# Kernel optimization log

Hardware: AMD Instinct MI355X
Metric: run time of the kernel (lower is better)

## Reference

```python
import jax, jax.numpy as jnp
import numpy as np

N_NODES = 100000
N_EDGES = 600000
IN_FEAT = 128
HID = 128
N_CLASSES = 64


def setup_inputs() -> dict:
    key = jax.random.key(0)
    ks = jax.random.split(key, 24)
    inp = {}
    inp["x"] = jax.random.normal(ks[0], (N_NODES, IN_FEAT), dtype=jnp.float32)
    for i, r in enumerate(["r0", "r1"]):
        inp[f"src_{r}"] = jax.random.randint(ks[1 + 3 * i], (N_EDGES,), 0, N_NODES, dtype=jnp.int32)
        inp[f"dst_{r}"] = jax.random.randint(ks[2 + 3 * i], (N_EDGES,), 0, N_NODES, dtype=jnp.int32)
        inp[f"ew_{r}"] = jax.random.uniform(ks[3 + 3 * i], (N_EDGES,), dtype=jnp.float32)
    def glorot(k, shape):
        fan = (shape[0] + shape[1]) / 2.0
        return jax.random.normal(k, shape, dtype=jnp.float32) / jnp.sqrt(fan)
    j = 7
    for r in ["r0", "r1"]:
        inp[f"Ws0_{r}"] = glorot(ks[j], (IN_FEAT, HID)); j += 1
        inp[f"Wn0_{r}"] = glorot(ks[j], (IN_FEAT, HID)); j += 1
        inp[f"b0_{r}"] = jnp.zeros((HID,), jnp.float32)
        inp[f"Wp_{r}"] = glorot(ks[j], (HID, HID)); j += 1
        inp[f"bp_{r}"] = jnp.zeros((HID,), jnp.float32)
        inp[f"Ws1_{r}"] = glorot(ks[j], (HID, N_CLASSES)); j += 1
        inp[f"Wn1_{r}"] = glorot(ks[j], (HID, N_CLASSES)); j += 1
        inp[f"b1_{r}"] = jnp.zeros((N_CLASSES,), jnp.float32)
    return inp


def _mean_agg(feat, src, dst, ew, n_nodes):
    # edge-weighted messages, mean over in-edges (divide by in-degree as DGL does)
    msg = feat[src] * ew[:, None]                      # [E, d]
    s = jax.ops.segment_sum(msg, dst, num_segments=n_nodes)
    deg = jax.ops.segment_sum(jnp.ones_like(ew), dst, num_segments=n_nodes)
    return s / jnp.maximum(deg, 1.0)[:, None]


def _max_agg(feat, src, dst, ew, n_nodes):
    msg = feat[src] * ew[:, None]                      # [E, d]
    m = jax.ops.segment_max(msg, dst, num_segments=n_nodes)
    deg = jax.ops.segment_sum(jnp.ones_like(ew), dst, num_segments=n_nodes)
    return jnp.where(deg[:, None] > 0, m, 0.0)         # zero for isolated nodes


def reference(x, src_r0, dst_r0, ew_r0, src_r1, dst_r1, ew_r1,
              Ws0_r0, Wn0_r0, b0_r0, Ws0_r1, Wn0_r1, b0_r1,
              Wp_r0, bp_r0, Ws1_r0, Wn1_r0, b1_r0,
              Wp_r1, bp_r1, Ws1_r1, Wn1_r1, b1_r1):
    n = x.shape[0]
    # Layer 0: per-relation SAGEConv(mean), HeteroGraphConv aggregate='sum', then relu
    h = jnp.zeros((n, Wn0_r0.shape[1]), x.dtype)
    for src, dst, ew, Ws, Wn, b in [
        (src_r0, dst_r0, ew_r0, Ws0_r0, Wn0_r0, b0_r0),
        (src_r1, dst_r1, ew_r1, Ws0_r1, Wn0_r1, b0_r1),
    ]:
        agg = _mean_agg(x, src, dst, ew, n)
        h = h + x @ Ws + agg @ Wn + b
    h = jax.nn.relu(h)
    # Classifier layer: per-relation SAGEConv(pool): relu(fc_pool(h_src)) -> max-agg
    logits = jnp.zeros((n, Wn1_r0.shape[1]), x.dtype)
    for src, dst, ew, Wp, bp, Ws, Wn, b in [
        (src_r0, dst_r0, ew_r0, Wp_r0, bp_r0, Ws1_r0, Wn1_r0, b1_r0),
        (src_r1, dst_r1, ew_r1, Wp_r1, bp_r1, Ws1_r1, Wn1_r1, b1_r1),
    ]:
        hp = jax.nn.relu(h @ Wp + bp)
        agg = _max_agg(hp, src, dst, ew, n)
        logits = logits + h @ Ws + agg @ Wn + b
    return logits
```

## Files before the change

kernel.cpp:

```cpp
#include <hip/hip_runtime.h>

typedef short bf16x8 __attribute__((ext_vector_type(8)));
typedef float f32x4 __attribute__((ext_vector_type(4)));
typedef unsigned short u16;
typedef unsigned int u32;

#define NN 100000
#define NE 600000
#define PART 12500
#define ECH 4688

__device__ __forceinline__ u16 f2b(float f) {
    u32 u = __float_as_uint(f);
    return (u16)((u + 0x7FFFu + ((u >> 16) & 1u)) >> 16);
}

__global__ void fused_setup(
    const float* __restrict__ x, u16* __restrict__ xo,
    const float* __restrict__ Ws0_0, const float* __restrict__ Ws0_1,
    const float* __restrict__ Wn0_0, const float* __restrict__ Wn0_1,
    const float* __restrict__ Wp_0,  const float* __restrict__ Wp_1,
    const float* __restrict__ Ws1_0, const float* __restrict__ Ws1_1,
    const float* __restrict__ Wn1_0, const float* __restrict__ Wn1_1,
    const float* __restrict__ b0_0, const float* __restrict__ b0_1,
    const float* __restrict__ b1_0, const float* __restrict__ b1_1,
    const float* __restrict__ bp_0, const float* __restrict__ bp_1,
    u16* __restrict__ w, float* __restrict__ bsum0, float* __restrict__ bsum1,
    float* __restrict__ bpc)
{
    int bb = blockIdx.x;
    if (bb < 12500) {
        int t = bb * 256 + threadIdx.x;
        const float4 v = reinterpret_cast<const float4*>(x)[t];
        ushort4 r; r.x = f2b(v.x); r.y = f2b(v.y); r.z = f2b(v.z); r.w = f2b(v.w);
        reinterpret_cast<ushort4*>(xo)[t] = r;
    } else {
        int t = (bb - 12500) * 256 + threadIdx.x;
        if (t < 81920) {
            int m = t >> 14, u = t & 16383;
            int n = u >> 7, k = u & 127;
            float v;
            if (m == 0)      v = Ws0_0[k * 128 + n] + Ws0_1[k * 128 + n];
            else if (m == 1) v = Wn0_0[k * 128 + n];
            else if (m == 2) v = Wn0_1[k * 128 + n];
            else if (m == 3) v = Wp_0[k * 128 + n];
            else             v = Wp_1[k * 128 + n];
            w[t] = f2b(v);
        } else if (t < 106496) {
            int u = t - 81920;
            int m = u >> 13; u &= 8191;
            int n = u >> 7, k = u & 127;
            float v;
            if (m == 0)      v = Ws1_0[k * 64 + n] + Ws1_1[k * 64 + n];
            else if (m == 1) v = Wn1_0[k * 64 + n];
            else             v = Wn1_1[k * 64 + n];
            w[t] = f2b(v);
        } else if (t < 106624) {
            int i = t - 106496; bsum0[i] = b0_0[i] + b0_1[i];
        } else if (t < 106688) {
            int i = t - 106624; bsum1[i] = b1_0[i] + b1_1[i];
        } else if (t < 106944) {
            int i = t - 106688; bpc[i] = (i < 128) ? bp_0[i] : bp_1[i - 128];
        }
    }
}

__global__ __launch_bounds__(256) void deg_part(
    const int* __restrict__ d0, const int* __restrict__ d1,
    int* __restrict__ g0, int* __restrict__ g1)
{
    int part = blockIdx.x & 7;
    int sub = blockIdx.x >> 3;
    int rel = sub & 1;
    int chunk = sub >> 1;
    const int lo = part * PART, hi = lo + PART;
    const int* d = rel ? d1 : d0;
    int* g = rel ? g1 : g0;
    const int e0 = chunk * ECH;
    const int e1 = min(e0 + ECH, NE);
    for (int e = e0 + threadIdx.x; e < e1; e += 256) {
        int dd = d[e];
        if (dd >= lo && dd < hi) atomicAdd(&g[dd], 1);
    }
}

__global__ void scan_local(const int* __restrict__ deg0, const int* __restrict__ deg1,
                           int* __restrict__ offs0, int* __restrict__ offs1,
                           int* __restrict__ bsA, int* __restrict__ bsB)
{
    __shared__ int sm[1024];
    int rel = blockIdx.x >= 98;
    int blk = blockIdx.x - rel * 98;
    const int* in = rel ? deg1 : deg0;
    int* out = rel ? offs1 : offs0;
    int* bsum = rel ? bsB : bsA;
    int t = threadIdx.x;
    int i = blk * 1024 + t;
    int v = (i < NN) ? in[i] : 0;
    sm[t] = v;
    __syncthreads();
    for (int off = 1; off < 1024; off <<= 1) {
        int add = (t >= off) ? sm[t - off] : 0;
        __syncthreads();
        sm[t] += add;
        __syncthreads();
    }
    if (i < NN) out[i] = sm[t] - v;
    if (t == 1023) bsum[blk] = sm[1023];
}

__global__ void scan_bsums(int* __restrict__ bsA, int* __restrict__ bsB)
{
    __shared__ int sm[128];
    int* bsum = blockIdx.x ? bsB : bsA;
    int t = threadIdx.x;
    int v = (t < 98) ? bsum[t] : 0;
    sm[t] = v;
    __syncthreads();
    for (int off = 1; off < 128; off <<= 1) {
        int add = (t >= off) ? sm[t - off] : 0;
        __syncthreads();
        sm[t] += add;
        __syncthreads();
    }
    if (t < 98) bsum[t] = sm[t] - v;
}

__global__ void scan_add(int* __restrict__ offs0, int* __restrict__ offs1,
                         const int* __restrict__ bsA, const int* __restrict__ bsB,
                         int* __restrict__ cur0, int* __restrict__ cur1,
                         u32* __restrict__ csr0, u32* __restrict__ csr1)
{
    int rel = blockIdx.x >= 392;
    int i = (blockIdx.x - rel * 392) * 256 + threadIdx.x;
    int* offs = rel ? offs1 : offs0;
    int* cur = rel ? cur1 : cur0;
    const int* bsum = rel ? bsB : bsA;
    if (i < NN) {
        int v = offs[i] + bsum[i >> 10];
        offs[i] = v;
        cur[i] = v;
    }
    if (i == 0) offs[NN] = NE;
    if (blockIdx.x == 0 && threadIdx.x < 8) {
        csr0[NE + threadIdx.x] = 0;
        csr1[NE + threadIdx.x] = 0;
    }
}

__global__ __launch_bounds__(256) void build_csr_part(
    const int* __restrict__ src0, const int* __restrict__ dst0,
    const float* __restrict__ ew0,
    const int* __restrict__ src1, const int* __restrict__ dst1,
    const float* __restrict__ ew1,
    int* __restrict__ cur0, int* __restrict__ cur1,
    u32* __restrict__ csr0, u32* __restrict__ csr1)
{
    int part = blockIdx.x & 7;
    int sub = blockIdx.x >> 3;
    int rel = sub & 1;
    int chunk = sub >> 1;
    const int lo = part * PART, hi = lo + PART;
    const int* src = rel ? src1 : src0;
    const int* dst = rel ? dst1 : dst0;
    const float* ew = rel ? ew1 : ew0;
    int* cur = rel ? cur1 : cur0;
    u32* csr = rel ? csr1 : csr0;
    const int e0 = chunk * ECH;
    const int e1 = min(e0 + ECH, NE);
    for (int e = e0 + threadIdx.x; e < e1; e += 256) {
        int d = dst[e];
        if (d >= lo && d < hi) {
            int p = atomicAdd(&cur[d], 1);
            u32 q = (u32)__float2int_rn(ew[e] * 32767.f);
            csr[p] = ((u32)src[e] << 15) | q;
        }
    }
}

template<bool MAXAGG>
__global__ __launch_bounds__(256) void gather(
    const u16* __restrict__ F0, const u16* __restrict__ F1,
    const int* __restrict__ offs0, const u32* __restrict__ csr0, u16* __restrict__ o0,
    const int* __restrict__ offs1, const u32* __restrict__ csr1, u16* __restrict__ o1)
{
    int b = blockIdx.x;
    int rel = b >= 25000;
    const u16* F = rel ? F1 : F0;
    const int* offs = rel ? offs1 : offs0;
    const u32* csr = rel ? csr1 : csr0;
    u16* out = rel ? o1 : o0;
    int node = (b - rel * 25000) * 4 + (threadIdx.x >> 6);
    int lane = threadIdx.x & 63;
    int beg = __builtin_amdgcn_readfirstlane(offs[node]);
    int end = __builtin_amdgcn_readfirstlane(offs[node + 1]);
    const u16* base = F + (lane << 1);

    float acc0[8], acc1[8];
#pragma unroll
    for (int i = 0; i < 8; ++i) { acc0[i] = 0.f; acc1[i] = 0.f; }

    for (int e = beg; e < end; e += 8) {
        u32 E[8];
        float wq[8];
#pragma unroll
        for (int i = 0; i < 8; ++i) E[i] = csr[e + i];
        wq[0] = (float)(E[0] & 0x7FFFu);
#pragma unroll
        for (int i = 1; i < 8; ++i)
            wq[i] = (e + i < end) ? (float)(E[i] & 0x7FFFu) : 0.f;
#pragma unroll
        for (int i = 0; i < 8; ++i) {
            u32 v = *reinterpret_cast<const u32*>(base + ((E[i] >> 15) << 7));
            float f0 = __uint_as_float(v << 16);
            float f1 = __uint_as_float(v & 0xFFFF0000u);
            if (MAXAGG) {
                acc0[i] = fmaxf(acc0[i], f0 * wq[i]);
                acc1[i] = fmaxf(acc1[i], f1 * wq[i]);
            } else {
                acc0[i] = fmaf(f0, wq[i], acc0[i]);
                acc1[i] = fmaf(f1, wq[i], acc1[i]);
            }
        }
    }

    float a0, a1, scale;
    if (MAXAGG) {
        a0 = fmaxf(fmaxf(fmaxf(acc0[0], acc0[1]), fmaxf(acc0[2], acc0[3])),
                   fmaxf(fmaxf(acc0[4], acc0[5]), fmaxf(acc0[6], acc0[7])));
        a1 = fmaxf(fmaxf(fmaxf(acc1[0], acc1[1]), fmaxf(acc1[2], acc1[3])),
                   fmaxf(fmaxf(acc1[4], acc1[5]), fmaxf(acc1[6], acc1[7])));
        scale = 1.f / 32767.f;
    } else {
        a0 = ((acc0[0] + acc0[1]) + (acc0[2] + acc0[3])) +
             ((acc0[4] + acc0[5]) + (acc0[6] + acc0[7]));
        a1 = ((acc1[0] + acc1[1]) + (acc1[2] + acc1[3])) +
             ((acc1[4] + acc1[5]) + (acc1[6] + acc1[7]));
        scale = 1.f / (32767.f * fmaxf((float)(end - beg), 1.f));
    }
    ushort2 r; r.x = f2b(a0 * scale); r.y = f2b(a1 * scale);
    *reinterpret_cast<ushort2*>(out + (size_t)node * 128 + (lane << 1)) = r;
}

template<int NPAIR, int COLGROUPS, int WAVES, bool RELU, bool OUTF32, bool DUAL>
__global__ __launch_bounds__(WAVES * 64, 2) void gemm_reg(
    const u16* __restrict__ A0, const u16* __restrict__ A1, const u16* __restrict__ A2,
    const u16* __restrict__ BT, const float* __restrict__ bias,
    float* __restrict__ outF, u16* __restrict__ outB, u16* __restrict__ outB2)
{
    constexpr int NC = COLGROUPS * 32;
    constexpr int RT = WAVES / COLGROUPS;
    constexpr int OST = DUAL ? (NC / 2) : NC;
    constexpr int NTILES = NN / 32;
    const int w = threadIdx.x >> 6, l = threadIdx.x & 63;
    const int cg = w % COLGROUPS, rsub = w / COLGROUPS;
    const int l15 = l & 15, lk = (l >> 4) << 3, rq = (l >> 4) << 2;

    bf16x8 bfr[NPAIR][4][2];
#pragma unroll
    for (int p = 0; p < NPAIR; ++p)
#pragma unroll
        for (int ks = 0; ks < 4; ++ks)
#pragma unroll
            for (int cf = 0; cf < 2; ++cf) {
                int n = p * NC + cg * 32 + cf * 16 + l15;
                bfr[p][ks][cf] = *reinterpret_cast<const bf16x8*>(BT + (size_t)n * 128 + ks * 32 + lk);
            }

    const u16* As[3] = {A0, A1, A2};
    const float bv0 = bias[cg * 32 + l15];
    const float bv1 = bias[cg * 32 + 16 + l15];

    for (int tile = blockIdx.x * RT + rsub; tile < NTILES; tile += gridDim.x * RT) {
        const size_t rowbase = (size_t)tile * 32;

        bf16x8 af[NPAIR][4][2];
#pragma unroll
        for (int p = 0; p < NPAIR; ++p) {
            const u16* A = As[p] + rowbase * 128;
#pragma unroll
            for (int ks = 0; ks < 4; ++ks) {
                const int k0 = ks * 32 + lk;
                af[p][ks][0] = *reinterpret_cast<const bf16x8*>(A + (size_t)l15 * 128 + k0);
                af[p][ks][1] = *reinterpret_cast<const bf16x8*>(A + (size_t)(16 + l15) * 128 + k0);
            }
        }

        f32x4 acc[2][2];
#pragma unroll
        for (int rf = 0; rf < 2; ++rf)
#pragma unroll
            for (int cf = 0; cf < 2; ++cf)
                acc[rf][cf] = f32x4{0.f, 0.f, 0.f, 0.f};

#pragma unroll
        for (int p = 0; p < NPAIR; ++p)
#pragma unroll
            for (int ks = 0; ks < 4; ++ks) {
                acc[0][0] = __builtin_amdgcn_mfma_f32_16x16x32_bf16(af[p][ks][0], bfr[p][ks][0], acc[0][0], 0, 0, 0);
                acc[0][1] = __builtin_amdgcn_mfma_f32_16x16x32_bf16(af[p][ks][0], bfr[p][ks][1], acc[0][1], 0, 0, 0);
                acc[1][0] = __builtin_amdgcn_mfma_f32_16x16x32_bf16(af[p][ks][1], bfr[p][ks][0], acc[1][0], 0, 0, 0);
                acc[1][1] = __builtin_amdgcn_mfma_f32_16x16x32_bf16(af[p][ks][1], bfr[p][ks][1], acc[1][1], 0, 0, 0);
            }

        u16* ob = outB;
        if (DUAL && cg >= 4) ob = outB2;
        const int colbase = (DUAL ? (cg & 3) : cg) * 32;
#pragma unroll
        for (int cf = 0; cf < 2; ++cf) {
            const int col = colbase + cf * 16 + l15;
            const float bv = cf ? bv1 : bv0;
#pragma unroll
            for (int rf = 0; rf < 2; ++rf) {
#pragma unroll
                for (int j = 0; j < 4; ++j) {
                    const size_t row = rowbase + rf * 16 + rq + j;
                    float v = acc[rf][cf][j] + bv;
                    if (RELU) v = fmaxf(v, 0.f);
                    if (OUTF32) outF[row * OST + col] = v;
                    else        ob[row * OST + col] = f2b(v);
                }
            }
        }
    }
}

extern "C" void kernel_launch(void* const* d_in, const int* in_sizes, int n_in,
                              void* d_out, int out_size, void* d_ws, size_t ws_size,
                              hipStream_t stream)
{
    const float* x     = (const float*)d_in[0];
    const int*   src0  = (const int*)d_in[1];
    const int*   dst0  = (const int*)d_in[2];
    const float* ew0   = (const float*)d_in[3];
    const int*   src1  = (const int*)d_in[4];
    const int*   dst1  = (const int*)d_in[5];
    const float* ew1   = (const float*)d_in[6];
    const float* Ws0_0 = (const float*)d_in[7];
    const float* Wn0_0 = (const float*)d_in[8];
    const float* b0_0  = (const float*)d_in[9];
    const float* Wp_0  = (const float*)d_in[10];
    const float* bp_0  = (const float*)d_in[11];
    const float* Ws1_0 = (const float*)d_in[12];
    const float* Wn1_0 = (const float*)d_in[13];
    const float* b1_0  = (const float*)d_in[14];
    const float* Ws0_1 = (const float*)d_in[15];
    const float* Wn0_1 = (const float*)d_in[16];
    const float* b0_1  = (const float*)d_in[17];
    const float* Wp_1  = (const float*)d_in[18];
    const float* bp_1  = (const float*)d_in[19];
    const float* Ws1_1 = (const float*)d_in[20];
    const float* Wn1_1 = (const float*)d_in[21];
    const float* b1_1  = (const float*)d_in[22];

    char* ws = (char*)d_ws;
    u16*   x16   = (u16*)(ws + 0);
    u16*   h16   = (u16*)(ws + 25600000);
    u16*   a0    = (u16*)(ws + 51200000);
    u16*   a1    = (u16*)(ws + 76800000);
    u16*   hp1   = (u16*)(ws + 102400000);
    u32*   csr0  = (u32*)(ws + 128000000);
    u32*   csr1  = (u32*)(ws + 130400032);
    int*   offs0 = (int*)(ws + 132800064);
    int*   offs1 = (int*)(ws + 133200080);
    int*   cur0  = (int*)(ws + 133600096);
    int*   cur1  = (int*)(ws + 134000096);
    int*   deg0  = (int*)(ws + 134400096);
    int*   deg1  = (int*)(ws + 134800096);
    int*   bsA   = (int*)(ws + 135200096);
    int*   bsB   = (int*)(ws + 135200608);
    u16*   wts   = (u16*)(ws + 135201120);
    float* bsum0 = (float*)(ws + 135414112);
    float* bsum1 = (float*)(ws + 135414624);
    float* bpc   = (float*)(ws + 135415136);

    u16* hp0 = x16;

    hipMemsetAsync(deg0, 0, 800000, stream);
    deg_part<<<2048, 256, 0, stream>>>(dst0, dst1, deg0, deg1);
    fused_setup<<<12918, 256, 0, stream>>>(
        x, x16, Ws0_0, Ws0_1, Wn0_0, Wn0_1, Wp_0, Wp_1,
        Ws1_0, Ws1_1, Wn1_0, Wn1_1, b0_0, b0_1, b1_0, b1_1, bp_0, bp_1,
        wts, bsum0, bsum1, bpc);

    scan_local<<<196, 1024, 0, stream>>>(deg0, deg1, offs0, offs1, bsA, bsB);
    scan_bsums<<<2, 128, 0, stream>>>(bsA, bsB);
    scan_add<<<784, 256, 0, stream>>>(offs0, offs1, bsA, bsB, cur0, cur1, csr0, csr1);
    build_csr_part<<<2048, 256, 0, stream>>>(
        src0, dst0, ew0, src1, dst1, ew1, cur0, cur1, csr0, csr1);

    gather<false><<<50000, 256, 0, stream>>>(x16, x16, offs0, csr0, a0, offs1, csr1, a1);
    gemm_reg<3, 4, 4, true, false, false><<<1024, 256, 0, stream>>>(
        x16, a0, a1, wts, bsum0, nullptr, h16, nullptr);

    gemm_reg<1, 8, 8, true, false, true><<<512, 512, 0, stream>>>(
        h16, nullptr, nullptr, wts + 49152, bpc, nullptr, hp0, hp1);
    gather<true><<<50000, 256, 0, stream>>>(hp0, hp1, offs0, csr0, a0, offs1, csr1, a1);
    gemm_reg<3, 2, 4, false, true, false><<<782, 256, 0, stream>>>(
        h16, a0, a1, wts + 81920, bsum1, (float*)d_out, nullptr, nullptr);
}
```

Measured before the change: 374.2 us.

## Software-pipeline gather with persistent waves and fold degree count into setup

Replaces the one-wave-per-node gather with persistent waves, each walking 25 nodes with a stride of 4096. Offsets, CSR entries and feature rows for upcoming nodes are prefetched into registers so loads overlap the current node's accumulation. The degree-count kernel is merged into the fused setup kernel to save a launch. Edge weights are now quantised by taking mantissa bits of the float directly instead of scaling to a 15-bit integer, which drops the rescale step. The trade-offs are higher register pressure and far fewer waves in flight, and the new weight encoding only holds for weights in [0,1).

```diff
diff --git a/kernel.cpp b/kernel.cpp
--- a/kernel.cpp
+++ b/kernel.cpp
@@ -9,6 +9,8 @@
 #define NE 600000
 #define PART 12500
 #define ECH 4688
+#define S 4096
+#define NSTEP 25
 
 __device__ __forceinline__ u16 f2b(float f) {
     u32 u = __float_as_uint(f);
@@ -26,16 +28,32 @@
     const float* __restrict__ b1_0, const float* __restrict__ b1_1,
     const float* __restrict__ bp_0, const float* __restrict__ bp_1,
     u16* __restrict__ w, float* __restrict__ bsum0, float* __restrict__ bsum1,
-    float* __restrict__ bpc)
+    float* __restrict__ bpc,
+    const int* __restrict__ d0, const int* __restrict__ d1,
+    int* __restrict__ g0, int* __restrict__ g1)
 {
     int bb = blockIdx.x;
-    if (bb < 12500) {
-        int t = bb * 256 + threadIdx.x;
+    if (bb < 2048) {
+        int part = bb & 7;
+        int sub = bb >> 3;
+        int rel = sub & 1;
+        int chunk = sub >> 1;
+        const int lo = part * PART, hi = lo + PART;
+        const int* d = rel ? d1 : d0;
+        int* g = rel ? g1 : g0;
+        const int e0 = chunk * ECH;
+        const int e1 = min(e0 + ECH, NE);
+        for (int e = e0 + threadIdx.x; e < e1; e += 256) {
+            int dd = d[e];
+            if (dd >= lo && dd < hi) atomicAdd(&g[dd], 1);
+        }
+    } else if (bb < 14548) {
+        int t = (bb - 2048) * 256 + threadIdx.x;
         const float4 v = reinterpret_cast<const float4*>(x)[t];
         ushort4 r; r.x = f2b(v.x); r.y = f2b(v.y); r.z = f2b(v.z); r.w = f2b(v.w);
         reinterpret_cast<ushort4*>(xo)[t] = r;
     } else {
-        int t = (bb - 12500) * 256 + threadIdx.x;
+        int t = (bb - 14548) * 256 + threadIdx.x;
         if (t < 81920) {
             int m = t >> 14, u = t & 16383;
             int n = u >> 7, k = u & 127;
@@ -65,25 +83,6 @@
     }
 }
 
-__global__ __launch_bounds__(256) void deg_part(
-    const int* __restrict__ d0, const int* __restrict__ d1,
-    int* __restrict__ g0, int* __restrict__ g1)
-{
-    int part = blockIdx.x & 7;
-    int sub = blockIdx.x >> 3;
-    int rel = sub & 1;
-    int chunk = sub >> 1;
-    const int lo = part * PART, hi = lo + PART;
-    const int* d = rel ? d1 : d0;
-    int* g = rel ? g1 : g0;
-    const int e0 = chunk * ECH;
-    const int e1 = min(e0 + ECH, NE);
-    for (int e = e0 + threadIdx.x; e < e1; e += 256) {
-        int dd = d[e];
-        if (dd >= lo && dd < hi) atomicAdd(&g[dd], 1);
-    }
-}
-
 __global__ void scan_local(const int* __restrict__ deg0, const int* __restrict__ deg1,
                            int* __restrict__ offs0, int* __restrict__ offs1,
                            int* __restrict__ bsA, int* __restrict__ bsB)
@@ -172,74 +171,84 @@
         int d = dst[e];
         if (d >= lo && d < hi) {
             int p = atomicAdd(&cur[d], 1);
-            u32 q = (u32)__float2int_rn(ew[e] * 32767.f);
+            u32 q = (__float_as_uint(ew[e]) + 0x10000u) >> 17;
             csr[p] = ((u32)src[e] << 15) | q;
         }
     }
 }
 
 template<bool MAXAGG>
-__global__ __launch_bounds__(256) void gather(
+__global__ __launch_bounds__(256) void gather_pipe(
     const u16* __restrict__ F0, const u16* __restrict__ F1,
     const int* __restrict__ offs0, const u32* __restrict__ csr0, u16* __restrict__ o0,
     const int* __restrict__ offs1, const u32* __restrict__ csr1, u16* __restrict__ o1)
 {
-    int b = blockIdx.x;
-    int rel = b >= 25000;
+    int wid = blockIdx.x * 4 + (threadIdx.x >> 6);
+    int rel = wid >= S;
+    int w0 = wid - rel * S;
     const u16* F = rel ? F1 : F0;
     const int* offs = rel ? offs1 : offs0;
     const u32* csr = rel ? csr1 : csr0;
     u16* out = rel ? o1 : o0;
-    int node = (b - rel * 25000) * 4 + (threadIdx.x >> 6);
-    int lane = threadIdx.x & 63;
-    int beg = __builtin_amdgcn_readfirstlane(offs[node]);
-    int end = __builtin_amdgcn_readfirstlane(offs[node + 1]);
-    const u16* base = F + (lane << 1);
-
-    float acc0[8], acc1[8];
-#pragma unroll
-    for (int i = 0; i < 8; ++i) { acc0[i] = 0.f; acc1[i] = 0.f; }
-
-    for (int e = beg; e < end; e += 8) {
-        u32 E[8];
-        float wq[8];
-#pragma unroll
-        for (int i = 0; i < 8; ++i) E[i] = csr[e + i];
-        wq[0] = (float)(E[0] & 0x7FFFu);
-#pragma unroll
-        for (int i = 1; i < 8; ++i)
-            wq[i] = (e + i < end) ? (float)(E[i] & 0x7FFFu) : 0.f;
-#pragma unroll
-        for (int i = 0; i < 8; ++i) {
-            u32 v = *reinterpret_cast<const u32*>(base + ((E[i] >> 15) << 7));
-            float f0 = __uint_as_float(v << 16);
-            float f1 = __uint_as_float(v & 0xFFFF0000u);
-            if (MAXAGG) {
-                acc0[i] = fmaxf(acc0[i], f0 * wq[i]);
-                acc1[i] = fmaxf(acc1[i], f1 * wq[i]);
-            } else {
-                acc0[i] = fmaf(f0, wq[i], acc0[i]);
-                acc1[i] = fmaf(f1, wq[i], acc1[i]);
+    const int lane2 = (threadIdx.x & 63) << 1;
+
+#define LDOFFS(n, b, c) { int nc_ = min((n), NN - 1); b = offs[nc_]; \
+                          c = ((n) < NN) ? (offs[nc_ + 1] - b) : 0; }
+#define LDCSR(dst, b, c) { int last_ = max((c) - 1, 0); \
+    _Pragma("unroll") for (int j = 0; j < 8; ++j) dst[j] = csr[(b) + min(j, last_)]; }
+#define LDTBL(dst, E) { _Pragma("unroll") for (int j = 0; j < 8; ++j) \
+    dst[j] = *reinterpret_cast<const u32*>(F + ((size_t)(E[j] >> 15) << 7) + lane2); }
+
+    int bC, cC, bN, cN, bF, cF;
+    u32 EC[8], EN[8], EF[8], vC[8], vN[8];
+    LDOFFS(w0,         bC, cC);
+    LDOFFS(w0 + S,     bN, cN);
+    LDOFFS(w0 + 2 * S, bF, cF);
+    LDCSR(EC, bC, cC);
+    LDCSR(EN, bN, cN);
+    LDTBL(vC, EC);
+
+    for (int it = 0; it < NSTEP; ++it) {
+        const int nC = w0 + it * S;
+        int bF2, cF2;
+        LDOFFS(nC + 3 * S, bF2, cF2);
+        LDCSR(EF, bF, cF);
+        LDTBL(vN, EN);
+
+        float a0 = 0.f, a1 = 0.f;
+#pragma unroll
+        for (int j = 0; j < 8; ++j) {
+            float wgt = (j < cC) ? __uint_as_float(EC[j] << 17) : 0.f;
+            float f0 = __uint_as_float(vC[j] << 16);
+            float f1 = __uint_as_float(vC[j] & 0xFFFF0000u);
+            if (MAXAGG) { a0 = fmaxf(a0, f0 * wgt); a1 = fmaxf(a1, f1 * wgt); }
+            else        { a0 = fmaf(f0, wgt, a0);   a1 = fmaf(f1, wgt, a1); }
+        }
+        for (int base = 8; base < cC; base += 8) {
+#pragma unroll
+            for (int j = 0; j < 8; ++j) {
+                int idx = min(base + j, cC - 1);
+                u32 E = csr[bC + idx];
+                u32 v = *reinterpret_cast<const u32*>(F + ((size_t)(E >> 15) << 7) + lane2);
+                float wgt = (base + j < cC) ? __uint_as_float(E << 17) : 0.f;
+                float f0 = __uint_as_float(v << 16);
+                float f1 = __uint_as_float(v & 0xFFFF0000u);
+                if (MAXAGG) { a0 = fmaxf(a0, f0 * wgt); a1 = fmaxf(a1, f1 * wgt); }
+                else        { a0 = fmaf(f0, wgt, a0);   a1 = fmaf(f1, wgt, a1); }
             }
         }
-    }
-
-    float a0, a1, scale;
-    if (MAXAGG) {
-        a0 = fmaxf(fmaxf(fmaxf(acc0[0], acc0[1]), fmaxf(acc0[2], acc0[3])),
-                   fmaxf(fmaxf(acc0[4], acc0[5]), fmaxf(acc0[6], acc0[7])));
-        a1 = fmaxf(fmaxf(fmaxf(acc1[0], acc1[1]), fmaxf(acc1[2], acc1[3])),
-                   fmaxf(fmaxf(acc1[4], acc1[5]), fmaxf(acc1[6], acc1[7])));
-        scale = 1.f / 32767.f;
-    } else {
-        a0 = ((acc0[0] + acc0[1]) + (acc0[2] + acc0[3])) +
-             ((acc0[4] + acc0[5]) + (acc0[6] + acc0[7]));
-        a1 = ((acc1[0] + acc1[1]) + (acc1[2] + acc1[3])) +
-             ((acc1[4] + acc1[5]) + (acc1[6] + acc1[7]));
-        scale = 1.f / (32767.f * fmaxf((float)(end - beg), 1.f));
-    }
-    ushort2 r; r.x = f2b(a0 * scale); r.y = f2b(a1 * scale);
-    *reinterpret_cast<ushort2*>(out + (size_t)node * 128 + (lane << 1)) = r;
+        if (nC < NN) {
+            float s = MAXAGG ? 1.f : 1.f / fmaxf((float)cC, 1.f);
+            ushort2 r; r.x = f2b(a0 * s); r.y = f2b(a1 * s);
+            *reinterpret_cast<ushort2*>(out + (size_t)nC * 128 + lane2) = r;
+        }
+        bC = bN; cC = cN; bN = bF; cN = cF; bF = bF2; cF = cF2;
+#pragma unroll
+        for (int j = 0; j < 8; ++j) { EC[j] = EN[j]; EN[j] = EF[j]; vC[j] = vN[j]; }
+    }
+#undef LDOFFS
+#undef LDCSR
+#undef LDTBL
 }
 
 template<int NPAIR, int COLGROUPS, int WAVES, bool RELU, bool OUTF32, bool DUAL>
@@ -377,11 +386,10 @@
     u16* hp0 = x16;
 
     hipMemsetAsync(deg0, 0, 800000, stream);
-    deg_part<<<2048, 256, 0, stream>>>(dst0, dst1, deg0, deg1);
-    fused_setup<<<12918, 256, 0, stream>>>(
+    fused_setup<<<14966, 256, 0, stream>>>(
         x, x16, Ws0_0, Ws0_1, Wn0_0, Wn0_1, Wp_0, Wp_1,
         Ws1_0, Ws1_1, Wn1_0, Wn1_1, b0_0, b0_1, b1_0, b1_1, bp_0, bp_1,
-        wts, bsum0, bsum1, bpc);
+        wts, bsum0, bsum1, bpc, dst0, dst1, deg0, deg1);
 
     scan_local<<<196, 1024, 0, stream>>>(deg0, deg1, offs0, offs1, bsA, bsB);
     scan_bsums<<<2, 128, 0, stream>>>(bsA, bsB);
@@ -389,13 +397,15 @@
     build_csr_part<<<2048, 256, 0, stream>>>(
         src0, dst0, ew0, src1, dst1, ew1, cur0, cur1, csr0, csr1);
 
-    gather<false><<<50000, 256, 0, stream>>>(x16, x16, offs0, csr0, a0, offs1, csr1, a1);
+    gather_pipe<false><<<2048, 256, 0, stream>>>(
+        x16, x16, offs0, csr0, a0, offs1, csr1, a1);
     gemm_reg<3, 4, 4, true, false, false><<<1024, 256, 0, stream>>>(
         x16, a0, a1, wts, bsum0, nullptr, h16, nullptr);
 
     gemm_reg<1, 8, 8, true, false, true><<<512, 512, 0, stream>>>(
         h16, nullptr, nullptr, wts + 49152, bpc, nullptr, hp0, hp1);
-    gather<true><<<50000, 256, 0, stream>>>(hp0, hp1, offs0, csr0, a0, offs1, csr1, a1);
+    gather_pipe<true><<<2048, 256, 0, stream>>>(
+        hp0, hp1, offs0, csr0, a0, offs1, csr1, a1);
     gemm_reg<3, 2, 4, false, true, false><<<782, 256, 0, stream>>>(
         h16, a0, a1, wts + 81920, bsum1, (float*)d_out, nullptr, nullptr);
 }
```

After: 405.5 us. 8.4% more time.
